# Optimization experiments

Measured on AMD Instinct MI355X. Metric: run time of the kernel, lower is better.

The kernel has to match this reference:

```python
import jax, jax.numpy as jnp
import numpy as np

MARGIN = 0.3
FAMILY_TABLE = jnp.array([0, 1, 2, 1, 3, 3], dtype=jnp.int32)  # num_classes == 6
_BIG = 1e9  # finite sentinel (avoids inf*0 NaNs under autodiff)
_EPS = 1e-12  # F.normalize eps


def setup_inputs() -> dict:
    key = jax.random.key(0)
    k1, k2 = jax.random.split(key)
    B, D = 8192, 64
    embeddings = jax.random.normal(k1, (B, D), dtype=jnp.float32)
    labels = jax.random.randint(k2, (B,), 0, 6, dtype=jnp.int64)
    return {"embeddings": embeddings, "labels": labels}


def reference(embeddings, labels):
    B = embeddings.shape[0]
    # fam[i] = family_table[labels[i]]; labels are always < len(table) here,
    # so no -1 entries occur (matches original semantics for in-range labels).
    fam = jnp.take(FAMILY_TABLE, labels)  # [B]

    # L2-normalize rows (F.normalize with eps clamp)
    norm = jnp.maximum(jnp.linalg.norm(embeddings, axis=-1, keepdims=True), _EPS)
    emb_norm = embeddings / norm

    # cosine distance matrix [B, B]
    dist = 1.0 - emb_norm @ emb_norm.T

    same = (fam[:, None] == fam[None, :]) & (~jnp.eye(B, dtype=bool))  # [B,B]
    diff = fam[:, None] != fam[None, :]                                 # [B,B]

    d_pos = jnp.max(jnp.where(same, dist, -_BIG), axis=1)  # hardest positive
    d_neg = jnp.min(jnp.where(diff, dist, _BIG), axis=1)   # hardest negative

    valid = same.any(axis=1) & diff.any(axis=1)  # rows contributing to loss
    per_row = jnp.where(valid, jax.nn.relu(d_pos - d_neg + MARGIN), 0.0)

    count = jnp.sum(valid.astype(jnp.float32))
    return jnp.sum(per_row) / jnp.maximum(count, 1.0)
```

## Files before the change

### kernel.cpp

```cpp
#include <hip/hip_runtime.h>
#include <math.h>

#define MARGIN 0.3f
#define NJ 32
#define NPAIR 8

typedef short bf16x8 __attribute__((ext_vector_type(8)));
typedef float f32x4 __attribute__((ext_vector_type(4)));
typedef unsigned int u32;
typedef const __attribute__((address_space(1))) u32* gp_t;
typedef __attribute__((address_space(3))) u32* lp_t;

__device__ __forceinline__ unsigned short f2bf_rne(float x) {
    unsigned b = __float_as_uint(x);
    unsigned r = b + 0x7FFFu + ((b >> 16) & 1u);
    return (unsigned short)(r >> 16);
}
__device__ __forceinline__ int fam_of(int lbl) { return (0xF64 >> (2 * lbl)) & 3; }

__global__ __launch_bounds__(256) void prep_kernel(
    const float* __restrict__ emb, const int* __restrict__ labels,
    unsigned char* __restrict__ famSorted, int* __restrict__ famLoHi,
    unsigned* __restrict__ counters, short* __restrict__ pack, int B) {
    __shared__ int wt[4][4];
    __shared__ int posL[32];
    const int t = threadIdx.x, lane = t & 63, wid = t >> 6, bid = blockIdx.x;

    unsigned long long lfp = 0ull;
    int lc0 = 0, lc1 = 0, lc2 = 0, lc3 = 0;
#pragma unroll
    for (int j = 0; j < 32; j++) {
        int f = fam_of(labels[t * 32 + j]);
        lfp |= (unsigned long long)f << (2 * j);
        lc0 += (f == 0); lc1 += (f == 1); lc2 += (f == 2); lc3 += (f == 3);
    }
    int i0 = lc0, i1 = lc1, i2 = lc2, i3 = lc3;
#pragma unroll
    for (int o = 1; o < 64; o <<= 1) {
        int u0 = __shfl_up(i0, o, 64), u1 = __shfl_up(i1, o, 64);
        int u2 = __shfl_up(i2, o, 64), u3 = __shfl_up(i3, o, 64);
        if (lane >= o) { i0 += u0; i1 += u1; i2 += u2; i3 += u3; }
    }
    if (lane == 63) { wt[wid][0] = i0; wt[wid][1] = i1; wt[wid][2] = i2; wt[wid][3] = i3; }
    __syncthreads();
    int wb0 = 0, wb1 = 0, wb2 = 0, wb3 = 0, to0 = 0, to1 = 0, to2 = 0, to3 = 0;
#pragma unroll
    for (int w2 = 0; w2 < 4; w2++) {
        int v0 = wt[w2][0], v1 = wt[w2][1], v2 = wt[w2][2], v3 = wt[w2][3];
        if (w2 < wid) { wb0 += v0; wb1 += v1; wb2 += v2; wb3 += v3; }
        to0 += v0; to1 += v1; to2 += v2; to3 += v3;
    }
    const int fb0 = 0, fb1 = to0, fb2 = to0 + to1, fb3 = to0 + to1 + to2;
    if (bid == 0 && t == 0) {
        famLoHi[0] = fb0; famLoHi[1] = fb1; famLoHi[2] = fb2; famLoHi[3] = fb3;
        famLoHi[4] = fb1; famLoHi[5] = fb2; famLoHi[6] = fb3; famLoHi[7] = fb3 + to3;
        counters[0] = 0;
    }
    int b0 = fb0 + wb0 + (i0 - lc0);
    int b1 = fb1 + wb1 + (i1 - lc1);
    int b2 = fb2 + wb2 + (i2 - lc2);
    int b3 = fb3 + wb3 + (i3 - lc3);
#pragma unroll
    for (int j = 0; j < 32; j++) {
        int f = (int)((lfp >> (2 * j)) & 3ull);
        int pos = (f == 0) ? b0 : ((f == 1) ? b1 : ((f == 2) ? b2 : b3));
        if (bid == 0) famSorted[pos] = (unsigned char)f;
        if (t == bid) posL[j] = pos;
        b0 += (f == 0); b1 += (f == 1); b2 += (f == 2); b3 += (f == 3);
    }
    __syncthreads();
#pragma unroll
    for (int rep = 0; rep < 8; rep++) {
        int rl = rep * 4 + wid;
        float x = emb[(size_t)(bid * 32 + rl) * 64 + lane];
        float ss = x * x;
#pragma unroll
        for (int o = 32; o > 0; o >>= 1) ss += __shfl_xor(ss, o, 64);
        unsigned short h = f2bf_rne(x / fmaxf(sqrtf(ss), 1e-12f));
        int pos = posL[rl];
        size_t idx = (size_t)(pos >> 4) * 1024 + (size_t)(lane >> 3) * 128 +
                     (size_t)(pos & 15) * 8 + (lane & 7);
        pack[idx] = (short)h;
    }
}

__global__ __launch_bounds__(256) void gemm_minmax_kernel(
    const short* __restrict__ pack,
    const unsigned char* __restrict__ famSorted, const int* __restrict__ famLoHi,
    float* __restrict__ pMin, float* __restrict__ pMax, int B) {
    __shared__ short ldsB[16384];

    const int lane = threadIdx.x & 63;
    const int wid  = threadIdx.x >> 6;
    const int g = lane >> 4;
    const int c = lane & 15;
    const int rowBase = blockIdx.x * 256 + wid * 64;
    const int aStrip0 = rowBase >> 4;
    const int jChunk0 = blockIdx.y * 256;
    const int jStrip0 = jChunk0 >> 4;

    bf16x8 aH[4][2];
#pragma unroll
    for (int s = 0; s < 4; s++) {
        const short* pA = pack + (size_t)(aStrip0 + s) * 1024;
        aH[s][0] = *(const bf16x8*)(pA + lane * 8);
        aH[s][1] = *(const bf16x8*)(pA + 512 + lane * 8);
    }

    {
        const char* src = (const char*)(pack + (size_t)jStrip0 * 1024);
#pragma unroll
        for (int i = 0; i < 8; i++) {
            int off = wid * 8192 + i * 1024;
            __builtin_amdgcn_global_load_lds((gp_t)(src + off + lane * 16),
                                             (lp_t)((char*)ldsB + off), 16, 0, 0);
        }
    }

    int sLo[4], sHi[4], sUni[4];
#pragma unroll
    for (int s = 0; s < 4; s++) {
        int f0  = famSorted[rowBase + s * 16];
        int f15 = famSorted[rowBase + s * 16 + 15];
        sUni[s] = __builtin_amdgcn_readfirstlane((f0 == f15) ? 1 : 0);
        sLo[s]  = __builtin_amdgcn_readfirstlane(famLoHi[f0]);
        sHi[s]  = __builtin_amdgcn_readfirstlane(famLoHi[4 + f0]);
    }

    const f32x4 zq = {0.f, 0.f, 0.f, 0.f};
    float mn[4] = {1e30f, 1e30f, 1e30f, 1e30f};
    float mx[4] = {-1e30f, -1e30f, -1e30f, -1e30f};

    __syncthreads();

#pragma unroll
    for (int jp = 0; jp < NPAIR; jp++) {
        const int j0 = jChunk0 + jp * 32;
        const short* pB0 = ldsB + (size_t)(2 * jp) * 1024;
        const short* pB1 = pB0 + 1024;
        bf16x8 b0h0 = *(const bf16x8*)(pB0 + lane * 8);
        bf16x8 b0h1 = *(const bf16x8*)(pB0 + 512 + lane * 8);
        bf16x8 b1h0 = *(const bf16x8*)(pB1 + lane * 8);
        bf16x8 b1h1 = *(const bf16x8*)(pB1 + 512 + lane * 8);

#pragma unroll
        for (int s = 0; s < 4; s++) {
            f32x4 accA, accB;
            accA = __builtin_amdgcn_mfma_f32_16x16x32_bf16(b0h0, aH[s][0], zq, 0, 0, 0);
            accB = __builtin_amdgcn_mfma_f32_16x16x32_bf16(b1h0, aH[s][0], zq, 0, 0, 0);
            accA = __builtin_amdgcn_mfma_f32_16x16x32_bf16(b0h1, aH[s][1], accA, 0, 0, 0);
            accB = __builtin_amdgcn_mfma_f32_16x16x32_bf16(b1h1, aH[s][1], accB, 0, 0, 0);

            if (sUni[s] && j0 >= sLo[s] && j0 + 32 <= sHi[s]) {
                float a01 = fminf(accA[0], accA[1]), a23 = fminf(accA[2], accA[3]);
                float b01 = fminf(accB[0], accB[1]), b23 = fminf(accB[2], accB[3]);
                mn[s] = fminf(mn[s], fminf(fminf(a01, a23), fminf(b01, b23)));
            } else if (sUni[s] && (j0 >= sHi[s] || j0 + 32 <= sLo[s])) {
                float a01 = fmaxf(accA[0], accA[1]), a23 = fmaxf(accA[2], accA[3]);
                float b01 = fmaxf(accB[0], accB[1]), b23 = fmaxf(accB[2], accB[3]);
                mx[s] = fmaxf(mx[s], fmaxf(fmaxf(a01, a23), fmaxf(b01, b23)));
            } else {
                int fi = famSorted[rowBase + s * 16 + c];
                unsigned fjA = *(const unsigned*)(famSorted + j0 + g * 4);
                unsigned fjB = *(const unsigned*)(famSorted + j0 + 16 + g * 4);
#pragma unroll
                for (int r = 0; r < 4; r++) {
                    bool sameA = ((int)((fjA >> (8 * r)) & 255u) == fi);
                    bool sameB = ((int)((fjB >> (8 * r)) & 255u) == fi);
                    mn[s] = fminf(mn[s], sameA ? accA[r] : 1e30f);
                    mx[s] = fmaxf(mx[s], sameA ? -1e30f : accA[r]);
                    mn[s] = fminf(mn[s], sameB ? accB[r] : 1e30f);
                    mx[s] = fmaxf(mx[s], sameB ? -1e30f : accB[r]);
                }
            }
        }
    }

#pragma unroll
    for (int s = 0; s < 4; s++) {
        float mnv = mn[s], mxv = mx[s];
        mnv = fminf(mnv, __shfl_xor(mnv, 16, 64));
        mxv = fmaxf(mxv, __shfl_xor(mxv, 16, 64));
        mnv = fminf(mnv, __shfl_xor(mnv, 32, 64));
        mxv = fmaxf(mxv, __shfl_xor(mxv, 32, 64));
        if (g == 0) {
            int row = rowBase + s * 16 + c;
            pMin[(size_t)blockIdx.y * B + row] = mnv;
            pMax[(size_t)blockIdx.y * B + row] = mxv;
        }
    }
}

__global__ __launch_bounds__(256) void rowloss_final_kernel(const float* __restrict__ pMin,
                                                            const float* __restrict__ pMax,
                                                            float* __restrict__ partial,
                                                            unsigned* __restrict__ counter,
                                                            float* __restrict__ out, int B) {
    const int nb = B / 256;
    const int row = blockIdx.x * 256 + threadIdx.x;
    float mn = 1e30f, mx = -1e30f;
#pragma unroll 8
    for (int cn = 0; cn < NJ; cn++) {
        mn = fminf(mn, pMin[(size_t)cn * B + row]);
        mx = fmaxf(mx, pMax[(size_t)cn * B + row]);
    }
    float sum = 0.f, cnt = 0.f;
    if (mn < 1e29f && mx > -1e29f) {
        sum = fmaxf(mx - mn + MARGIN, 0.f);
        cnt = 1.f;
    }
#pragma unroll
    for (int o = 32; o > 0; o >>= 1) {
        sum += __shfl_xor(sum, o, 64);
        cnt += __shfl_xor(cnt, o, 64);
    }
    __shared__ float sS[4], sC[4];
    const int lane = threadIdx.x & 63, w = threadIdx.x >> 6;
    if (lane == 0) { sS[w] = sum; sC[w] = cnt; }
    __syncthreads();
    if (threadIdx.x == 0) {
        partial[blockIdx.x]      = sS[0] + sS[1] + sS[2] + sS[3];
        partial[64 + blockIdx.x] = sC[0] + sC[1] + sC[2] + sC[3];
        __threadfence();
        unsigned done = atomicAdd(counter, 1u);
        if (done == (unsigned)(nb - 1)) {
            __threadfence();
            float S = 0.f, C = 0.f;
            for (int i = 0; i < nb; i++) { S += partial[i]; C += partial[64 + i]; }
            out[0] = S / fmaxf(C, 1.f);
        }
    }
}

extern "C" void kernel_launch(void* const* d_in, const int* in_sizes, int n_in,
                              void* d_out, int out_size, void* d_ws, size_t ws_size,
                              hipStream_t stream) {
    const float* emb    = (const float*)d_in[0];
    const int*   labels = (const int*)d_in[1];
    const int B = in_sizes[1];

    char* base = (char*)d_ws;
    size_t off = 0;
    auto alloc = [&](size_t bytes) -> char* {
        char* p = base + off;
        off = (off + bytes + 255) & ~(size_t)255;
        return p;
    };
    unsigned char* famSorted = (unsigned char*)alloc((size_t)B);
    int*           famLoHi   = (int*)alloc(64);
    unsigned*      counters  = (unsigned*)alloc(64);
    short*         pack      = (short*)alloc((size_t)B * 64 * 2);
    float*         pMin      = (float*)alloc((size_t)NJ * B * 4);
    float*         pMax      = (float*)alloc((size_t)NJ * B * 4);
    float*         partial   = (float*)alloc(128 * 4);

    prep_kernel<<<256, 256, 0, stream>>>(emb, labels, famSorted, famLoHi,
                                         counters, pack, B);
    dim3 g3(B / 256, NJ);
    gemm_minmax_kernel<<<g3, 256, 0, stream>>>(pack, famSorted, famLoHi, pMin, pMax, B);
    rowloss_final_kernel<<<B / 256, 256, 0, stream>>>(pMin, pMax, partial, counters,
                                                      (float*)d_out, B);
}
```

Measured before the change: 32.05 us.

## Loop each GEMM block over four column chunks with double-buffered LDS prefetch

Each gemm block now covers 1024 columns instead of 256. It walks four 256-column chunks and prefetches the next chunk into a second LDS buffer with async global-to-LDS loads while computing on the current one. This cuts the grid from 32 column groups to 8, which shrinks the pMin/pMax partial buffers and the reduction work in the final kernel, and reuses the register-resident A fragments across more columns. In exchange there are far fewer blocks (roughly one per CU), 64KB of LDS per block and a barrier per chunk, which can lower occupancy and latency hiding.

After: 43.64 us. 36.2% more time.

```diff
diff --git a/kernel.cpp b/kernel.cpp
--- a/kernel.cpp
+++ b/kernel.cpp
@@ -2,8 +2,7 @@
 #include <math.h>
 
 #define MARGIN 0.3f
-#define NJ 32
-#define NPAIR 8
+#define NJG 8
 
 typedef short bf16x8 __attribute__((ext_vector_type(8)));
 typedef float f32x4 __attribute__((ext_vector_type(4)));
@@ -88,7 +87,7 @@
     const short* __restrict__ pack,
     const unsigned char* __restrict__ famSorted, const int* __restrict__ famLoHi,
     float* __restrict__ pMin, float* __restrict__ pMax, int B) {
-    __shared__ short ldsB[16384];
+    __shared__ short ldsB[32768];
 
     const int lane = threadIdx.x & 63;
     const int wid  = threadIdx.x >> 6;
@@ -96,8 +95,8 @@
     const int c = lane & 15;
     const int rowBase = blockIdx.x * 256 + wid * 64;
     const int aStrip0 = rowBase >> 4;
-    const int jChunk0 = blockIdx.y * 256;
-    const int jStrip0 = jChunk0 >> 4;
+    const int colGroup = blockIdx.y;
+    const int jGroup0 = colGroup * 1024;
 
     bf16x8 aH[4][2];
 #pragma unroll
@@ -108,7 +107,7 @@
     }
 
     {
-        const char* src = (const char*)(pack + (size_t)jStrip0 * 1024);
+        const char* src = (const char*)(pack + (size_t)(jGroup0 >> 4) * 1024);
 #pragma unroll
         for (int i = 0; i < 8; i++) {
             int off = wid * 8192 + i * 1024;
@@ -133,47 +132,63 @@
 
     __syncthreads();
 
-#pragma unroll
-    for (int jp = 0; jp < NPAIR; jp++) {
-        const int j0 = jChunk0 + jp * 32;
-        const short* pB0 = ldsB + (size_t)(2 * jp) * 1024;
-        const short* pB1 = pB0 + 1024;
-        bf16x8 b0h0 = *(const bf16x8*)(pB0 + lane * 8);
-        bf16x8 b0h1 = *(const bf16x8*)(pB0 + 512 + lane * 8);
-        bf16x8 b1h0 = *(const bf16x8*)(pB1 + lane * 8);
-        bf16x8 b1h1 = *(const bf16x8*)(pB1 + 512 + lane * 8);
-
-#pragma unroll
-        for (int s = 0; s < 4; s++) {
-            f32x4 accA, accB;
-            accA = __builtin_amdgcn_mfma_f32_16x16x32_bf16(b0h0, aH[s][0], zq, 0, 0, 0);
-            accB = __builtin_amdgcn_mfma_f32_16x16x32_bf16(b1h0, aH[s][0], zq, 0, 0, 0);
-            accA = __builtin_amdgcn_mfma_f32_16x16x32_bf16(b0h1, aH[s][1], accA, 0, 0, 0);
-            accB = __builtin_amdgcn_mfma_f32_16x16x32_bf16(b1h1, aH[s][1], accB, 0, 0, 0);
-
-            if (sUni[s] && j0 >= sLo[s] && j0 + 32 <= sHi[s]) {
-                float a01 = fminf(accA[0], accA[1]), a23 = fminf(accA[2], accA[3]);
-                float b01 = fminf(accB[0], accB[1]), b23 = fminf(accB[2], accB[3]);
-                mn[s] = fminf(mn[s], fminf(fminf(a01, a23), fminf(b01, b23)));
-            } else if (sUni[s] && (j0 >= sHi[s] || j0 + 32 <= sLo[s])) {
-                float a01 = fmaxf(accA[0], accA[1]), a23 = fmaxf(accA[2], accA[3]);
-                float b01 = fmaxf(accB[0], accB[1]), b23 = fmaxf(accB[2], accB[3]);
-                mx[s] = fmaxf(mx[s], fmaxf(fmaxf(a01, a23), fmaxf(b01, b23)));
-            } else {
-                int fi = famSorted[rowBase + s * 16 + c];
-                unsigned fjA = *(const unsigned*)(famSorted + j0 + g * 4);
-                unsigned fjB = *(const unsigned*)(famSorted + j0 + 16 + g * 4);
-#pragma unroll
-                for (int r = 0; r < 4; r++) {
-                    bool sameA = ((int)((fjA >> (8 * r)) & 255u) == fi);
-                    bool sameB = ((int)((fjB >> (8 * r)) & 255u) == fi);
-                    mn[s] = fminf(mn[s], sameA ? accA[r] : 1e30f);
-                    mx[s] = fmaxf(mx[s], sameA ? -1e30f : accA[r]);
-                    mn[s] = fminf(mn[s], sameB ? accB[r] : 1e30f);
-                    mx[s] = fmaxf(mx[s], sameB ? -1e30f : accB[r]);
+    for (int ch = 0; ch < 4; ch++) {
+        const int jChunk0 = jGroup0 + ch * 256;
+        const char* bufC = (char*)ldsB + (ch & 1) * 32768;
+        if (ch < 3) {
+            const char* src = (const char*)(pack + (size_t)((jChunk0 + 256) >> 4) * 1024);
+            const char* dst = (char*)ldsB + ((ch + 1) & 1) * 32768;
+#pragma unroll
+            for (int i = 0; i < 8; i++) {
+                int off = wid * 8192 + i * 1024;
+                __builtin_amdgcn_global_load_lds((gp_t)(src + off + lane * 16),
+                                                 (lp_t)(dst + off), 16, 0, 0);
+            }
+        }
+
+#pragma unroll
+        for (int jp = 0; jp < 8; jp++) {
+            const int j0 = jChunk0 + jp * 32;
+            const short* pB0 = (const short*)bufC + (size_t)(2 * jp) * 1024;
+            const short* pB1 = pB0 + 1024;
+            bf16x8 b0h0 = *(const bf16x8*)(pB0 + lane * 8);
+            bf16x8 b0h1 = *(const bf16x8*)(pB0 + 512 + lane * 8);
+            bf16x8 b1h0 = *(const bf16x8*)(pB1 + lane * 8);
+            bf16x8 b1h1 = *(const bf16x8*)(pB1 + 512 + lane * 8);
+
+#pragma unroll
+            for (int s = 0; s < 4; s++) {
+                f32x4 accA, accB;
+                accA = __builtin_amdgcn_mfma_f32_16x16x32_bf16(b0h0, aH[s][0], zq, 0, 0, 0);
+                accB = __builtin_amdgcn_mfma_f32_16x16x32_bf16(b1h0, aH[s][0], zq, 0, 0, 0);
+                accA = __builtin_amdgcn_mfma_f32_16x16x32_bf16(b0h1, aH[s][1], accA, 0, 0, 0);
+                accB = __builtin_amdgcn_mfma_f32_16x16x32_bf16(b1h1, aH[s][1], accB, 0, 0, 0);
+
+                if (sUni[s] && j0 >= sLo[s] && j0 + 32 <= sHi[s]) {
+                    float a01 = fminf(accA[0], accA[1]), a23 = fminf(accA[2], accA[3]);
+                    float b01 = fminf(accB[0], accB[1]), b23 = fminf(accB[2], accB[3]);
+                    mn[s] = fminf(mn[s], fminf(fminf(a01, a23), fminf(b01, b23)));
+                } else if (sUni[s] && (j0 >= sHi[s] || j0 + 32 <= sLo[s])) {
+                    float a01 = fmaxf(accA[0], accA[1]), a23 = fmaxf(accA[2], accA[3]);
+                    float b01 = fmaxf(accB[0], accB[1]), b23 = fmaxf(accB[2], accB[3]);
+                    mx[s] = fmaxf(mx[s], fmaxf(fmaxf(a01, a23), fmaxf(b01, b23)));
+                } else {
+                    int fi = famSorted[rowBase + s * 16 + c];
+                    unsigned fjA = *(const unsigned*)(famSorted + j0 + g * 4);
+                    unsigned fjB = *(const unsigned*)(famSorted + j0 + 16 + g * 4);
+#pragma unroll
+                    for (int r = 0; r < 4; r++) {
+                        bool sameA = ((int)((fjA >> (8 * r)) & 255u) == fi);
+                        bool sameB = ((int)((fjB >> (8 * r)) & 255u) == fi);
+                        mn[s] = fminf(mn[s], sameA ? accA[r] : 1e30f);
+                        mx[s] = fmaxf(mx[s], sameA ? -1e30f : accA[r]);
+                        mn[s] = fminf(mn[s], sameB ? accB[r] : 1e30f);
+                        mx[s] = fmaxf(mx[s], sameB ? -1e30f : accB[r]);
+                    }
                 }
             }
         }
+        __syncthreads();
     }
 
 #pragma unroll
@@ -185,8 +200,8 @@
         mxv = fmaxf(mxv, __shfl_xor(mxv, 32, 64));
         if (g == 0) {
             int row = rowBase + s * 16 + c;
-            pMin[(size_t)blockIdx.y * B + row] = mnv;
-            pMax[(size_t)blockIdx.y * B + row] = mxv;
+            pMin[(size_t)colGroup * B + row] = mnv;
+            pMax[(size_t)colGroup * B + row] = mxv;
         }
     }
 }
@@ -199,8 +214,8 @@
     const int nb = B / 256;
     const int row = blockIdx.x * 256 + threadIdx.x;
     float mn = 1e30f, mx = -1e30f;
-#pragma unroll 8
-    for (int cn = 0; cn < NJ; cn++) {
+#pragma unroll
+    for (int cn = 0; cn < NJG; cn++) {
         mn = fminf(mn, pMin[(size_t)cn * B + row]);
         mx = fmaxf(mx, pMax[(size_t)cn * B + row]);
     }
@@ -250,13 +265,13 @@
     int*           famLoHi   = (int*)alloc(64);
     unsigned*      counters  = (unsigned*)alloc(64);
     short*         pack      = (short*)alloc((size_t)B * 64 * 2);
-    float*         pMin      = (float*)alloc((size_t)NJ * B * 4);
-    float*         pMax      = (float*)alloc((size_t)NJ * B * 4);
+    float*         pMin      = (float*)alloc((size_t)NJG * B * 4);
+    float*         pMax      = (float*)alloc((size_t)NJG * B * 4);
     float*         partial   = (float*)alloc(128 * 4);
 
     prep_kernel<<<256, 256, 0, stream>>>(emb, labels, famSorted, famLoHi,
                                          counters, pack, B);
-    dim3 g3(B / 256, NJ);
+    dim3 g3(B / 256, NJG);
     gemm_minmax_kernel<<<g3, 256, 0, stream>>>(pack, famSorted, famLoHi, pMin, pMax, B);
     rowloss_final_kernel<<<B / 256, 256, 0, stream>>>(pMin, pMax, partial, counters,
                                                       (float*)d_out, B);
```

## Halve column chunk per block and remap 1D grid with XCD-aware swizzle

Applied to the files above, without the earlier changes.

The column chunk per GEMM block drops from 256 to 128 and the partial-result count doubles, so the launch has 2048 blocks instead of 1024 and each block uses half the LDS. The 2D grid becomes a 1D grid with a swizzled block-to-(row, column) mapping. The mapping appears meant to group blocks that share column data on the same XCD and improve L2 reuse. In exchange, each block amortises its A-fragment loads over less work, and the final reduction reads twice as many partial min/max values per row.

After: 35.30 us. +10.2%, slower.

```diff
diff --git a/kernel.cpp b/kernel.cpp
--- a/kernel.cpp
+++ b/kernel.cpp
@@ -2,8 +2,8 @@
 #include <math.h>
 
 #define MARGIN 0.3f
-#define NJ 32
-#define NPAIR 8
+#define NJ 64
+#define NPAIR 4
 
 typedef short bf16x8 __attribute__((ext_vector_type(8)));
 typedef float f32x4 __attribute__((ext_vector_type(4)));
@@ -88,15 +88,19 @@
     const short* __restrict__ pack,
     const unsigned char* __restrict__ famSorted, const int* __restrict__ famLoHi,
     float* __restrict__ pMin, float* __restrict__ pMax, int B) {
-    __shared__ short ldsB[16384];
+    __shared__ short ldsB[8192];
 
     const int lane = threadIdx.x & 63;
     const int wid  = threadIdx.x >> 6;
     const int g = lane >> 4;
     const int c = lane & 15;
-    const int rowBase = blockIdx.x * 256 + wid * 64;
+    const int bid = blockIdx.x;
+    const int r = bid & 7, q = bid >> 3;
+    const int colBlock = r * 8 + (q & 7);
+    const int rowBlock = q >> 3;
+    const int rowBase = rowBlock * 256 + wid * 64;
     const int aStrip0 = rowBase >> 4;
-    const int jChunk0 = blockIdx.y * 256;
+    const int jChunk0 = colBlock * 128;
     const int jStrip0 = jChunk0 >> 4;
 
     bf16x8 aH[4][2];
@@ -110,8 +114,8 @@
     {
         const char* src = (const char*)(pack + (size_t)jStrip0 * 1024);
 #pragma unroll
-        for (int i = 0; i < 8; i++) {
-            int off = wid * 8192 + i * 1024;
+        for (int i = 0; i < 4; i++) {
+            int off = wid * 4096 + i * 1024;
             __builtin_amdgcn_global_load_lds((gp_t)(src + off + lane * 16),
                                              (lp_t)((char*)ldsB + off), 16, 0, 0);
         }
@@ -164,13 +168,13 @@
                 unsigned fjA = *(const unsigned*)(famSorted + j0 + g * 4);
                 unsigned fjB = *(const unsigned*)(famSorted + j0 + 16 + g * 4);
 #pragma unroll
-                for (int r = 0; r < 4; r++) {
-                    bool sameA = ((int)((fjA >> (8 * r)) & 255u) == fi);
-                    bool sameB = ((int)((fjB >> (8 * r)) & 255u) == fi);
-                    mn[s] = fminf(mn[s], sameA ? accA[r] : 1e30f);
-                    mx[s] = fmaxf(mx[s], sameA ? -1e30f : accA[r]);
-                    mn[s] = fminf(mn[s], sameB ? accB[r] : 1e30f);
-                    mx[s] = fmaxf(mx[s], sameB ? -1e30f : accB[r]);
+                for (int r2 = 0; r2 < 4; r2++) {
+                    bool sameA = ((int)((fjA >> (8 * r2)) & 255u) == fi);
+                    bool sameB = ((int)((fjB >> (8 * r2)) & 255u) == fi);
+                    mn[s] = fminf(mn[s], sameA ? accA[r2] : 1e30f);
+                    mx[s] = fmaxf(mx[s], sameA ? -1e30f : accA[r2]);
+                    mn[s] = fminf(mn[s], sameB ? accB[r2] : 1e30f);
+                    mx[s] = fmaxf(mx[s], sameB ? -1e30f : accB[r2]);
                 }
             }
         }
@@ -185,8 +189,8 @@
         mxv = fmaxf(mxv, __shfl_xor(mxv, 32, 64));
         if (g == 0) {
             int row = rowBase + s * 16 + c;
-            pMin[(size_t)blockIdx.y * B + row] = mnv;
-            pMax[(size_t)blockIdx.y * B + row] = mxv;
+            pMin[(size_t)colBlock * B + row] = mnv;
+            pMax[(size_t)colBlock * B + row] = mxv;
         }
     }
 }
@@ -256,8 +260,8 @@
 
     prep_kernel<<<256, 256, 0, stream>>>(emb, labels, famSorted, famLoHi,
                                          counters, pack, B);
-    dim3 g3(B / 256, NJ);
-    gemm_minmax_kernel<<<g3, 256, 0, stream>>>(pack, famSorted, famLoHi, pMin, pMax, B);
+    gemm_minmax_kernel<<<2048, 256, 0, stream>>>(pack, famSorted, famLoHi,
+                                                 pMin, pMax, B);
     rowloss_final_kernel<<<B / 256, 256, 0, stream>>>(pMin, pMax, partial, counters,
                                                       (float*)d_out, B);
 }
```
